# Optimization experiments

Measured on AMD Instinct MI355X. Metric: run time of the kernel, lower is better.

## Reference

```python
import jax, jax.numpy as jnp
import numpy as np
import math

S = 5   # num_states
D = 16  # observation_dim
F = 4   # transition_feature_dim
H = 2 * S  # transition net hidden


def setup_inputs() -> dict:
    key = jax.random.key(0)
    ks = jax.random.split(key, 10)
    B, T = 256, 4096
    observations = jax.random.normal(ks[0], (B, T, D), dtype=jnp.float32)
    transition_features = jax.random.normal(ks[1], (B, T, F), dtype=jnp.float32)
    # GaussianEmission params
    means = jax.random.normal(ks[2], (S, D), dtype=jnp.float32) * 0.1
    log_vars = jnp.zeros((S, D), dtype=jnp.float32)
    # HMM params
    log_initial = jnp.zeros((S,), dtype=jnp.float32)
    transition_bias = (jnp.eye(S) * 2.0 + jnp.ones((S, S)) * 0.1).astype(jnp.float32)
    # per-source-state transition nets: Linear(F,H)-Tanh-Linear(H,S)
    W1 = jax.random.normal(ks[3], (S, H, F), dtype=jnp.float32) * (1.0 / math.sqrt(F))
    b1 = jnp.zeros((S, H), dtype=jnp.float32)
    W2 = jax.random.normal(ks[4], (S, S, H), dtype=jnp.float32) * (1.0 / math.sqrt(H))
    b2 = jnp.zeros((S, S), dtype=jnp.float32)
    return {
        "observations": observations,
        "transition_features": transition_features,
        "means": means,
        "log_vars": log_vars,
        "log_initial": log_initial,
        "transition_bias": transition_bias,
        "W1": W1, "b1": b1, "W2": W2, "b2": b2,
    }


def _emission_log_prob(obs, means, log_vars):
    # diagonal Gaussian, expanded quadratic form to avoid [B,T,S,D] intermediate
    inv_v = jnp.exp(-log_vars)                              # [S,D]
    quad = (
        jnp.einsum('btd,sd->bts', obs * obs, inv_v)
        - 2.0 * jnp.einsum('btd,sd->bts', obs, means * inv_v)
        + jnp.sum(means * means * inv_v, axis=-1)           # [S]
    )
    const = D * math.log(2 * math.pi) + jnp.sum(log_vars, axis=-1)  # [S]
    return -0.5 * (const + quad)                            # [B,T,S]


def _io_log_transitions(feat, W1, b1, W2, b2, transition_bias):
    # feat: [B,T,F] -> log transition matrices [B,T,S,S] (row i = source state)
    h = jnp.tanh(jnp.einsum('btf,ihf->btih', feat, W1) + b1)        # [B,T,S,H]
    logits = jnp.einsum('btih,ioh->btio', h, W2) + b2 + transition_bias  # [B,T,S,S]
    probs = jax.nn.softmax(logits, axis=-1)
    return jnp.log(probs + 1e-10)


def reference(observations, transition_features, means, log_vars,
              log_initial, transition_bias, W1, b1, W2, b2):
    log_emis = _emission_log_prob(observations, means, log_vars)    # [B,T,S]
    log_init = jax.nn.log_softmax(log_initial)                      # [S]
    alpha0 = log_init + log_emis[:, 0, :]                           # [B,S]

    # transitions used at steps t=1..T-1
    log_trans = _io_log_transitions(transition_features[:, 1:], W1, b1, W2, b2,
                                    transition_bias)                # [B,T-1,S,S]

    lt_tm = jnp.swapaxes(log_trans, 0, 1)                           # [T-1,B,S,S]
    le_tm = jnp.swapaxes(log_emis[:, 1:, :], 0, 1)                  # [T-1,B,S]

    def step(alpha, xs):
        lt, le = xs
        alpha_new = jax.nn.logsumexp(alpha[:, :, None] + lt, axis=1) + le
        return alpha_new, alpha_new

    alpha_T, alphas = jax.lax.scan(step, alpha0, (lt_tm, le_tm))
    all_alpha = jnp.concatenate([alpha0[None], alphas], axis=0)     # [T,B,S]
    all_alpha = jnp.swapaxes(all_alpha, 0, 1)                       # [B,T,S]
    log_likelihood = jax.nn.logsumexp(alpha_T, axis=-1)             # [B]
    return log_likelihood, all_alpha
```

## Files before the change

kernel.cpp:

```cpp
#include <hip/hip_runtime.h>
#include <math.h>


namespace {

constexpr int kS = 5, kD = 16, kH = 10, kB = 256, kT = 4096;
constexpr int kC = 8, kNC = 512, kTile = 128, kCPT = 16, kG = 16, kNG = 32;

constexpr float kL2E = 1.4426950408889634f;
constexpr float kLn2 = 0.6931471805599453f;

constexpr int L_EA = 0;
constexpr int L_EB = 80;
constexpr int L_EC = 160;
constexpr int L_LN = 168;
constexpr int L_W1 = 176;
constexpr int L_B1 = 376;
constexpr int L_W2 = 436;
constexpr int L_B2 = 736;
constexpr int L_LV = 776;
constexpr int L_MN = 856;
constexpr int kPRM = 936;

__device__ __forceinline__ float max5(float a0, float a1, float a2, float a3, float a4) {
  return fmaxf(fmaxf(fmaxf(a0, a1), fmaxf(a2, a3)), a4);
}

__device__ __forceinline__ void loadObs(const float* __restrict__ obs_bt, float o[kD]) {
  const float4* o4 = reinterpret_cast<const float4*>(obs_bt);
  float4 v0 = o4[0], v1 = o4[1], v2 = o4[2], v3 = o4[3];
  o[0] = v0.x; o[1] = v0.y; o[2] = v0.z; o[3] = v0.w;
  o[4] = v1.x; o[5] = v1.y; o[6] = v1.z; o[7] = v1.w;
  o[8] = v2.x; o[9] = v2.y; o[10] = v2.z; o[11] = v2.w;
  o[12] = v3.x; o[13] = v3.y; o[14] = v3.z; o[15] = v3.w;
}

__device__ __forceinline__ unsigned bf16bits(float x) {
  unsigned u = __float_as_uint(x);
  return (u + 0x7fffu + ((u >> 16) & 1u)) >> 16;
}

__device__ void load_params(float* p, const float* means, const float* lvg,
                            const float* linit, const float* tbias,
                            const float* W1g, const float* b1g,
                            const float* W2g, const float* b2g) {
  const int tid = threadIdx.x, nt = blockDim.x;
  for (int i = tid; i < 80; i += nt) p[L_LV + i] = lvg[i];
  for (int i = tid; i < 80; i += nt) p[L_MN + i] = means[i];
  for (int i = tid; i < 200; i += nt) p[L_W1 + i] = (2.0f * kL2E) * W1g[i];
  for (int i = tid; i < 60; i += nt) {
    int r = i / 12, h = i - r * 12;
    p[L_B1 + i] = (h < kH) ? (2.0f * kL2E) * b1g[r * kH + h] : 0.f;
  }
  for (int i = tid; i < 300; i += nt) {
    int r = i / 12, h = i - r * 12;
    p[L_W2 + i] = (h < kH) ? kL2E * W2g[r * kH + h] : 0.f;
  }
  for (int i = tid; i < 40; i += nt) {
    int r = i / 8, j = i - r * 8;
    p[L_B2 + i] = (j < kS) ? kL2E * (b2g[r * kS + j] + tbias[r * kS + j]) : 0.f;
  }
  if (tid < kS) {
    float l0 = linit[0], l1 = linit[1], l2 = linit[2], l3 = linit[3], l4 = linit[4];
    float m = max5(l0, l1, l2, l3, l4);
    float se = __expf(l0 - m) + __expf(l1 - m) + __expf(l2 - m) +
               __expf(l3 - m) + __expf(l4 - m);
    p[L_LN + tid] = kL2E * (linit[tid] - (m + __logf(se)));
  }
  __syncthreads();
  for (int i = tid; i < 80; i += nt) {
    float iv = __expf(-p[L_LV + i]);
    p[L_EA + i] = -0.5f * kL2E * iv;
    p[L_EB + i] = kL2E * p[L_MN + i] * iv;
  }
  if (tid < kS) {
    float acc = 29.406033062549525f;
#pragma unroll
    for (int d = 0; d < 16; ++d) {
      float lvv = p[L_LV + tid * 16 + d], mm = p[L_MN + tid * 16 + d];
      acc += lvv + mm * mm * __expf(-lvv);
    }
    p[L_EC + tid] = -0.5f * kL2E * acc;
  }
  __syncthreads();
}

__device__ __forceinline__ void buildE(const float* __restrict__ obs,
                                       const float* __restrict__ feat,
                                       const float* __restrict__ p,
                                       size_t bt, float E[25], float& c) {
  float o[16];
  loadObs(obs + bt * kD, o);
  float le[5];
#pragma unroll
  for (int s = 0; s < 5; ++s) {
    float acc = p[L_EC + s];
#pragma unroll
    for (int d = 0; d < 16; ++d)
      acc = fmaf(o[d], fmaf(o[d], p[L_EA + s * 16 + d], p[L_EB + s * 16 + d]), acc);
    le[s] = acc;
  }
  c = max5(le[0], le[1], le[2], le[3], le[4]);
  float eml[5];
#pragma unroll
  for (int j = 0; j < 5; ++j) eml[j] = exp2f(le[j] - c);
  const float4 f = *reinterpret_cast<const float4*>(feat + bt * 4);
#pragma unroll
  for (int i = 0; i < 5; ++i) {
    float hv[10];
#pragma unroll
    for (int h = 0; h < 10; ++h) {
      float4 w = *reinterpret_cast<const float4*>(p + L_W1 + (i * 10 + h) * 4);
      float acc = p[L_B1 + i * 12 + h];
      acc = fmaf(f.x, w.x, acc); acc = fmaf(f.y, w.y, acc);
      acc = fmaf(f.z, w.z, acc); acc = fmaf(f.w, w.w, acc);
      float e = exp2f(acc);
      hv[h] = 1.f - 2.f * __builtin_amdgcn_rcpf(e + 1.f);
    }
    float eg[5], se = 0.f;
#pragma unroll
    for (int j = 0; j < 5; ++j) {
      const float* wr = p + L_W2 + (i * 5 + j) * 12;
      float4 w0 = *reinterpret_cast<const float4*>(wr);
      float4 w1 = *reinterpret_cast<const float4*>(wr + 4);
      float2 w2 = *reinterpret_cast<const float2*>(wr + 8);
      float acc = p[L_B2 + i * 8 + j];
      acc = fmaf(hv[0], w0.x, acc); acc = fmaf(hv[1], w0.y, acc);
      acc = fmaf(hv[2], w0.z, acc); acc = fmaf(hv[3], w0.w, acc);
      acc = fmaf(hv[4], w1.x, acc); acc = fmaf(hv[5], w1.y, acc);
      acc = fmaf(hv[6], w1.z, acc); acc = fmaf(hv[7], w1.w, acc);
      acc = fmaf(hv[8], w2.x, acc); acc = fmaf(hv[9], w2.y, acc);
      eg[j] = exp2f(acc);
      se += eg[j];
    }
    float rs = __builtin_amdgcn_rcpf(se);
#pragma unroll
    for (int j = 0; j < 5; ++j) E[i * 5 + j] = eg[j] * rs * eml[j];
  }
}

__device__ __forceinline__ void buildE0(const float* __restrict__ obs,
                                        const float* __restrict__ p, int b,
                                        float E[25], float& c) {
  float o[16];
  loadObs(obs + (size_t)b * kT * kD, o);
  float v[5];
#pragma unroll
  for (int s = 0; s < 5; ++s) {
    float acc = p[L_EC + s];
#pragma unroll
    for (int d = 0; d < 16; ++d)
      acc = fmaf(o[d], fmaf(o[d], p[L_EA + s * 16 + d], p[L_EB + s * 16 + d]), acc);
    v[s] = acc + p[L_LN + s];
  }
  c = max5(v[0], v[1], v[2], v[3], v[4]);
  float e[5];
#pragma unroll
  for (int j = 0; j < 5; ++j) e[j] = 0.2f * exp2f(v[j] - c);
#pragma unroll
  for (int i = 0; i < 5; ++i)
#pragma unroll
    for (int j = 0; j < 5; ++j) E[i * 5 + j] = e[j];
}

template <bool STORE_E>
__global__ __launch_bounds__(kTile, 4) void k_build(
    const float* __restrict__ obs, const float* __restrict__ feat,
    const float* __restrict__ means, const float* __restrict__ lv,
    const float* __restrict__ linit, const float* __restrict__ tbias,
    const float* __restrict__ W1g, const float* __restrict__ b1g,
    const float* __restrict__ W2g, const float* __restrict__ b2g,
    float* __restrict__ Rg, uint4* __restrict__ wsE) {
  __shared__ __align__(16) float p[kPRM];
  __shared__ float sw[kTile * 32];
  load_params(p, means, lv, linit, tbias, W1g, b1g, W2g, b2g);
  const int b = blockIdx.y, tile = blockIdx.x, tid = threadIdx.x;
  const int t = tile * kTile + tid;
  float E[25], c;
  if (t == 0) buildE0(obs, p, b, E, c);
  else buildE(obs, feat, p, (size_t)b * kT + t, E, c);
  if (STORE_E) {
    unsigned d[16];
#pragma unroll
    for (int q = 0; q < 12; ++q)
      d[q] = bf16bits(E[2 * q]) | (bf16bits(E[2 * q + 1]) << 16);
    unsigned cb = __float_as_uint(c);
    d[12] = bf16bits(E[24]) | (cb << 16);
    d[13] = cb >> 16;
    d[14] = 0; d[15] = 0;
    uint4* wp = wsE + ((size_t)b * kT + t) * 4;
#pragma unroll
    for (int q = 0; q < 4; ++q)
      wp[q] = make_uint4(d[4 * q], d[4 * q + 1], d[4 * q + 2], d[4 * q + 3]);
  }
  {
    const int base = tid * 32;
    const int off = (tid >> 3) + ((tid & 3) << 3);
#pragma unroll
    for (int e = 0; e < 25; ++e) sw[base + ((off + e) & 31)] = E[e];
    sw[base + ((off + 25) & 31)] = c;
  }
  __syncthreads();
  const int chunk = tid >> 3, ri = tid & 7;
  float R[5], sc;
  {
    const int base = (chunk * 8) * 32, off = chunk;
#pragma unroll
    for (int m = 0; m < 5; ++m) R[m] = sw[base + ((off + ri * 5 + m) & 31)];
    sc = sw[base + ((off + 25) & 31)];
  }
#pragma unroll 1
  for (int k = 1; k < 8; ++k) {
    const int base = (chunk * 8 + k) * 32, off = chunk + ((k & 3) << 3);
    float Ek[25];
#pragma unroll
    for (int e = 0; e < 25; ++e) Ek[e] = sw[base + ((off + e) & 31)];
    sc += sw[base + ((off + 25) & 31)];
    float nR[5];
#pragma unroll
    for (int j = 0; j < 5; ++j) {
      float acc = R[0] * Ek[j];
      acc = fmaf(R[1], Ek[5 + j], acc);
      acc = fmaf(R[2], Ek[10 + j], acc);
      acc = fmaf(R[3], Ek[15 + j], acc);
      acc = fmaf(R[4], Ek[20 + j], acc);
      nR[j] = acc;
    }
#pragma unroll
    for (int j = 0; j < 5; ++j) R[j] = nR[j];
    if ((k & 1) == 0 || k == 7) {
      float rm = (ri < 5) ? max5(R[0], R[1], R[2], R[3], R[4]) : 0.f;
      rm = fmaxf(rm, __shfl_xor(rm, 1, 8));
      rm = fmaxf(rm, __shfl_xor(rm, 2, 8));
      rm = fmaxf(rm, __shfl_xor(rm, 4, 8));
      rm = fmaxf(rm, 1e-37f);
      const float r = __builtin_amdgcn_rcpf(rm);
#pragma unroll
      for (int j = 0; j < 5; ++j) R[j] *= r;
      sc += __log2f(rm);
    }
  }
  if (ri < 5) {
    float* outr = Rg + ((size_t)b * kNC + tile * kCPT + chunk) * 28 + ri * 5;
#pragma unroll
    for (int m = 0; m < 5; ++m) outr[m] = R[m];
    if (ri == 0) outr[25] = sc;
  }
}

__global__ __launch_bounds__(256) void k_scan(const float* __restrict__ Rg,
                                              float* __restrict__ start,
                                              float* __restrict__ out) {
  __shared__ float sR[kNC * 32];
  __shared__ float sP[kNG * 28];
  __shared__ float sA[kNG * 8];
  const int b = blockIdx.x, tid = threadIdx.x;
#pragma unroll
  for (int r = 0; r < 2; ++r) {
    const int rec = r * 256 + tid;
    const float4* src = reinterpret_cast<const float4*>(Rg + ((size_t)b * kNC + rec) * 28);
    float4 q[7];
#pragma unroll
    for (int i = 0; i < 7; ++i) q[i] = src[i];
    const float* v = reinterpret_cast<const float*>(q);
    const int base = rec * 32, off = rec + (rec >> 4);
#pragma unroll
    for (int e = 0; e < 26; ++e) sR[base + ((off + e) & 31)] = v[e];
  }
  __syncthreads();
  if (tid < kNG) {
    const int g = tid;
    float P[25], psc;
    {
      const int rec = g * kG, base = rec * 32, off = rec + (rec >> 4);
#pragma unroll
      for (int e = 0; e < 25; ++e) P[e] = sR[base + ((off + e) & 31)];
      psc = sR[base + ((off + 25) & 31)];
    }
#pragma unroll 1
    for (int k = 1; k < kG; ++k) {
      const int rec = g * kG + k, base = rec * 32, off = rec + (rec >> 4);
      float M[25];
#pragma unroll
      for (int e = 0; e < 25; ++e) M[e] = sR[base + ((off + e) & 31)];
      psc += sR[base + ((off + 25) & 31)];
      float o[25];
#pragma unroll
      for (int i = 0; i < 5; ++i)
#pragma unroll
        for (int j = 0; j < 5; ++j) {
          float acc = P[i * 5 + 0] * M[j];
          acc = fmaf(P[i * 5 + 1], M[5 + j], acc);
          acc = fmaf(P[i * 5 + 2], M[10 + j], acc);
          acc = fmaf(P[i * 5 + 3], M[15 + j], acc);
          acc = fmaf(P[i * 5 + 4], M[20 + j], acc);
          o[i * 5 + j] = acc;
        }
#pragma unroll
      for (int e = 0; e < 25; ++e) P[e] = o[e];
      if (k & 1) {
        float m = P[0];
#pragma unroll
        for (int e = 1; e < 25; ++e) m = fmaxf(m, P[e]);
        m = fmaxf(m, 1e-37f);
        const float r = __builtin_amdgcn_rcpf(m);
#pragma unroll
        for (int e = 0; e < 25; ++e) P[e] *= r;
        psc += __log2f(m);
      }
    }
#pragma unroll
    for (int e = 0; e < 25; ++e) sP[g * 28 + e] = P[e];
    sP[g * 28 + 25] = psc;
  }
  __syncthreads();
  if (tid == 0) {
    float a[5] = {1.f, 1.f, 1.f, 1.f, 1.f};
    float ls = 0.f;
#pragma unroll 1
    for (int g = 0; g < kNG; ++g) {
#pragma unroll
      for (int s = 0; s < 5; ++s) sA[g * 8 + s] = a[s];
      sA[g * 8 + 5] = ls;
      float o[5];
#pragma unroll
      for (int j = 0; j < 5; ++j) {
        float acc = a[0] * sP[g * 28 + j];
        acc = fmaf(a[1], sP[g * 28 + 5 + j], acc);
        acc = fmaf(a[2], sP[g * 28 + 10 + j], acc);
        acc = fmaf(a[3], sP[g * 28 + 15 + j], acc);
        acc = fmaf(a[4], sP[g * 28 + 20 + j], acc);
        o[j] = acc;
      }
      ls += sP[g * 28 + 25];
      float m = fmaxf(max5(o[0], o[1], o[2], o[3], o[4]), 1e-37f);
      const float r = __builtin_amdgcn_rcpf(m);
#pragma unroll
      for (int j = 0; j < 5; ++j) a[j] = o[j] * r;
      ls += __log2f(m);
    }
    out[b] = (__log2f(a[0] + a[1] + a[2] + a[3] + a[4]) + ls) * kLn2;
  }
  __syncthreads();
  if (tid < kNG) {
    const int g = tid;
    float a[5], ls;
#pragma unroll
    for (int s = 0; s < 5; ++s) a[s] = sA[g * 8 + s];
    ls = sA[g * 8 + 5];
#pragma unroll 1
    for (int k = 0; k < kG; ++k) {
      const int cc = g * kG + k;
      float* st = start + ((size_t)b * kNC + cc) * 8;
      reinterpret_cast<float4*>(st)[0] = make_float4(a[0], a[1], a[2], a[3]);
      reinterpret_cast<float4*>(st)[1] = make_float4(a[4], ls, 0.f, 0.f);
      const int base = cc * 32, off = cc + (cc >> 4);
      float M[25];
#pragma unroll
      for (int e = 0; e < 25; ++e) M[e] = sR[base + ((off + e) & 31)];
      ls += sR[base + ((off + 25) & 31)];
      float o[5];
#pragma unroll
      for (int j = 0; j < 5; ++j) {
        float acc = a[0] * M[j];
        acc = fmaf(a[1], M[5 + j], acc);
        acc = fmaf(a[2], M[10 + j], acc);
        acc = fmaf(a[3], M[15 + j], acc);
        acc = fmaf(a[4], M[20 + j], acc);
        o[j] = acc;
      }
      float m = fmaxf(max5(o[0], o[1], o[2], o[3], o[4]), 1e-37f);
      const float r = __builtin_amdgcn_rcpf(m);
#pragma unroll
      for (int j = 0; j < 5; ++j) a[j] = o[j] * r;
      ls += __log2f(m);
    }
  }
}

__global__ __launch_bounds__(256) void k_alpha_a(const uint4* __restrict__ wsE,
                                                 const float* __restrict__ start,
                                                 float* __restrict__ outp) {
  const int g = blockIdx.x * 256 + threadIdx.x;
  const int b = g >> 9, cc = g & (kNC - 1);
  const float* st = start + (size_t)g * 8;
  const float4 s0 = reinterpret_cast<const float4*>(st)[0];
  float a[5] = {s0.x, s0.y, s0.z, s0.w, st[4]};
  float ls = st[5];
  float ov[40];
  const uint4* ep = wsE + ((size_t)b * kT + (size_t)cc * kC) * 4;
#pragma unroll
  for (int k = 0; k < 8; ++k) {
    uint4 q0 = ep[k * 4], q1 = ep[k * 4 + 1], q2 = ep[k * 4 + 2], q3 = ep[k * 4 + 3];
    unsigned d[14] = {q0.x, q0.y, q0.z, q0.w, q1.x, q1.y, q1.z, q1.w,
                      q2.x, q2.y, q2.z, q2.w, q3.x, q3.y};
    float E[25];
#pragma unroll
    for (int q = 0; q < 12; ++q) {
      E[2 * q]     = __uint_as_float(d[q] << 16);
      E[2 * q + 1] = __uint_as_float(d[q] & 0xffff0000u);
    }
    E[24] = __uint_as_float(d[12] << 16);
    const float cst = __uint_as_float((d[12] >> 16) | (d[13] << 16));
    float o[5];
#pragma unroll
    for (int j = 0; j < 5; ++j) {
      float acc = a[0] * E[j];
      acc = fmaf(a[1], E[5 + j], acc);
      acc = fmaf(a[2], E[10 + j], acc);
      acc = fmaf(a[3], E[15 + j], acc);
      acc = fmaf(a[4], E[20 + j], acc);
      o[j] = acc;
    }
    ls += cst;
    float L[5];
#pragma unroll
    for (int j = 0; j < 5; ++j) L[j] = __log2f(o[j]);
#pragma unroll
    for (int j = 0; j < 5; ++j) ov[k * 5 + j] = (L[j] + ls) * kLn2;
    const float lm = max5(L[0], L[1], L[2], L[3], L[4]);
    const float m = fmaxf(max5(o[0], o[1], o[2], o[3], o[4]), 1e-37f);
    const float r = __builtin_amdgcn_rcpf(m);
#pragma unroll
    for (int j = 0; j < 5; ++j) a[j] = o[j] * r;
    ls += lm;
  }
  float4* w = reinterpret_cast<float4*>(outp + kB + ((size_t)b * kT + (size_t)cc * kC) * kS);
#pragma unroll
  for (int q = 0; q < 10; ++q)
    w[q] = make_float4(ov[q * 4], ov[q * 4 + 1], ov[q * 4 + 2], ov[q * 4 + 3]);
}

__global__ __launch_bounds__(kTile, 4) void k_alpha_b(
    const float* __restrict__ obs, const float* __restrict__ feat,
    const float* __restrict__ means, const float* __restrict__ lv,
    const float* __restrict__ linit, const float* __restrict__ tbias,
    const float* __restrict__ W1g, const float* __restrict__ b1g,
    const float* __restrict__ W2g, const float* __restrict__ b2g,
    const float* __restrict__ start, float* __restrict__ outp) {
  __shared__ __align__(16) float p[kPRM];
  __shared__ float sw[kTile * 32];
  load_params(p, means, lv, linit, tbias, W1g, b1g, W2g, b2g);
  const int b = blockIdx.y, tile = blockIdx.x, tid = threadIdx.x;
  const int t = tile * kTile + tid;
  float E[25], c;
  if (t == 0) buildE0(obs, p, b, E, c);
  else buildE(obs, feat, p, (size_t)b * kT + t, E, c);
  {
    const int base = tid * 32;
    const int off = (tid >> 3) + ((tid & 3) << 3);
#pragma unroll
    for (int e = 0; e < 25; ++e) sw[base + ((off + e) & 31)] = E[e];
    sw[base + ((off + 25) & 31)] = c;
  }
  __syncthreads();
  if (tid < kCPT) {
    const int chunk = tid;
    const float* st = start + ((size_t)b * kNC + tile * kCPT + chunk) * 8;
    const float4 s0 = reinterpret_cast<const float4*>(st)[0];
    float a[5] = {s0.x, s0.y, s0.z, s0.w, st[4]};
    float ls = st[5];
    float ov[40];
#pragma unroll
    for (int k = 0; k < 8; ++k) {
      const int base = (chunk * 8 + k) * 32, off = chunk + ((k & 3) << 3);
      float Ek[25];
#pragma unroll
      for (int e = 0; e < 25; ++e) Ek[e] = sw[base + ((off + e) & 31)];
      const float cst = sw[base + ((off + 25) & 31)];
      float o[5];
#pragma unroll
      for (int j = 0; j < 5; ++j) {
        float acc = a[0] * Ek[j];
        acc = fmaf(a[1], Ek[5 + j], acc);
        acc = fmaf(a[2], Ek[10 + j], acc);
        acc = fmaf(a[3], Ek[15 + j], acc);
        acc = fmaf(a[4], Ek[20 + j], acc);
        o[j] = acc;
      }
      ls += cst;
      float L[5];
#pragma unroll
      for (int j = 0; j < 5; ++j) L[j] = __log2f(o[j]);
#pragma unroll
      for (int j = 0; j < 5; ++j) ov[k * 5 + j] = (L[j] + ls) * kLn2;
      const float lm = max5(L[0], L[1], L[2], L[3], L[4]);
      const float m = fmaxf(max5(o[0], o[1], o[2], o[3], o[4]), 1e-37f);
      const float r = __builtin_amdgcn_rcpf(m);
#pragma unroll
      for (int j = 0; j < 5; ++j) a[j] = o[j] * r;
      ls += lm;
    }
    float4* w = reinterpret_cast<float4*>(
        outp + kB + ((size_t)b * kT + (size_t)(tile * kCPT + chunk) * kC) * kS);
#pragma unroll
    for (int q = 0; q < 10; ++q)
      w[q] = make_float4(ov[q * 4], ov[q * 4 + 1], ov[q * 4 + 2], ov[q * 4 + 3]);
  }
}

}

extern "C" void kernel_launch(void* const* d_in, const int* in_sizes, int n_in,
                              void* d_out, int out_size, void* d_ws, size_t ws_size,
                              hipStream_t stream) {
  (void)in_sizes; (void)n_in; (void)out_size;
  const float* obs   = (const float*)d_in[0];
  const float* feat  = (const float*)d_in[1];
  const float* means = (const float*)d_in[2];
  const float* lv    = (const float*)d_in[3];
  const float* linit = (const float*)d_in[4];
  const float* tbias = (const float*)d_in[5];
  const float* W1g   = (const float*)d_in[6];
  const float* b1g   = (const float*)d_in[7];
  const float* W2g   = (const float*)d_in[8];
  const float* b2g   = (const float*)d_in[9];
  float* out = (float*)d_out;

  float* ws = (float*)d_ws;
  float* Rg    = ws;
  float* start = Rg + (size_t)kB * kNC * 28;
  uint4* wsE   = reinterpret_cast<uint4*>(start + (size_t)kB * kNC * 8);
  const size_t needA = (size_t)kB * kNC * 28 * 4 + (size_t)kB * kNC * 8 * 4 +
                       (size_t)kB * kT * 64;
  const bool useA = ws_size >= needA;

  dim3 gridB(kT / kTile, kB);
  if (useA) {
    k_build<true><<<gridB, kTile, 0, stream>>>(obs, feat, means, lv, linit, tbias,
                                               W1g, b1g, W2g, b2g, Rg, wsE);
  } else {
    k_build<false><<<gridB, kTile, 0, stream>>>(obs, feat, means, lv, linit, tbias,
                                                W1g, b1g, W2g, b2g, Rg, wsE);
  }
  k_scan<<<kB, 256, 0, stream>>>(Rg, start, out);
  if (useA) {
    k_alpha_a<<<(kB * kNC) / 256, 256, 0, stream>>>(wsE, start, out);
  } else {
    k_alpha_b<<<gridB, kTile, 0, stream>>>(obs, feat, means, lv, linit, tbias,
                                           W1g, b1g, W2g, b2g, start, out);
  }
}
```

Before: 135.1 us.

## Precompute parameters in a prep kernel, enlarge build tiles, simplify tanh MLP

Adds a one-block prep kernel that folds the emission constants, network weights and biases into a packed parameter buffer. Each build block then copies this buffer into shared memory instead of recomputing it with several syncs. The build tile grows from 128 to 256 threads. The tanh is rewritten as a reciprocal with the constant folded into the second-layer bias, the emission quadratic uses vectorised loads, and bf16 packing uses a hardware convert instruction. The fallback path that did not store E is removed, so the code now assumes the workspace is large enough, and one extra kernel launch is added.

```diff
diff --git a/kernel.cpp b/kernel.cpp
--- a/kernel.cpp
+++ b/kernel.cpp
@@ -4,29 +4,29 @@
 
 namespace {
 
-constexpr int kS = 5, kD = 16, kH = 10, kB = 256, kT = 4096;
-constexpr int kC = 8, kNC = 512, kTile = 128, kCPT = 16, kG = 16, kNG = 32;
+constexpr int kS = 5, kD = 16, kB = 256, kT = 4096;
+constexpr int kC = 8, kNC = 512;
+constexpr int kTile = 256, kCPT = 32;
+constexpr int kG = 16, kNG = 32;
 
 constexpr float kL2E = 1.4426950408889634f;
 constexpr float kLn2 = 0.6931471805599453f;
 
-constexpr int L_EA = 0;
-constexpr int L_EB = 80;
-constexpr int L_EC = 160;
+constexpr int L_QA = 0;
+constexpr int L_QB = 80;
+constexpr int L_QC = 160;
 constexpr int L_LN = 168;
 constexpr int L_W1 = 176;
 constexpr int L_B1 = 376;
 constexpr int L_W2 = 436;
-constexpr int L_B2 = 736;
-constexpr int L_LV = 776;
-constexpr int L_MN = 856;
-constexpr int kPRM = 936;
+constexpr int P_TOT = 768;
+constexpr int P_RSV = 1024;
 
 __device__ __forceinline__ float max5(float a0, float a1, float a2, float a3, float a4) {
   return fmaxf(fmaxf(fmaxf(a0, a1), fmaxf(a2, a3)), a4);
 }
 
-__device__ __forceinline__ void loadObs(const float* __restrict__ obs_bt, float o[kD]) {
+__device__ __forceinline__ void loadObs(const float* __restrict__ obs_bt, float* o) {
   const float4* o4 = reinterpret_cast<const float4*>(obs_bt);
   float4 v0 = o4[0], v1 = o4[1], v2 = o4[2], v3 = o4[3];
   o[0] = v0.x; o[1] = v0.y; o[2] = v0.z; o[3] = v0.w;
@@ -40,100 +40,121 @@
   return (u + 0x7fffu + ((u >> 16) & 1u)) >> 16;
 }
 
-__device__ void load_params(float* p, const float* means, const float* lvg,
-                            const float* linit, const float* tbias,
-                            const float* W1g, const float* b1g,
-                            const float* W2g, const float* b2g) {
-  const int tid = threadIdx.x, nt = blockDim.x;
-  for (int i = tid; i < 80; i += nt) p[L_LV + i] = lvg[i];
-  for (int i = tid; i < 80; i += nt) p[L_MN + i] = means[i];
-  for (int i = tid; i < 200; i += nt) p[L_W1 + i] = (2.0f * kL2E) * W1g[i];
-  for (int i = tid; i < 60; i += nt) {
-    int r = i / 12, h = i - r * 12;
-    p[L_B1 + i] = (h < kH) ? (2.0f * kL2E) * b1g[r * kH + h] : 0.f;
-  }
-  for (int i = tid; i < 300; i += nt) {
-    int r = i / 12, h = i - r * 12;
-    p[L_W2 + i] = (h < kH) ? kL2E * W2g[r * kH + h] : 0.f;
-  }
-  for (int i = tid; i < 40; i += nt) {
-    int r = i / 8, j = i - r * 8;
-    p[L_B2 + i] = (j < kS) ? kL2E * (b2g[r * kS + j] + tbias[r * kS + j]) : 0.f;
-  }
-  if (tid < kS) {
-    float l0 = linit[0], l1 = linit[1], l2 = linit[2], l3 = linit[3], l4 = linit[4];
-    float m = max5(l0, l1, l2, l3, l4);
-    float se = __expf(l0 - m) + __expf(l1 - m) + __expf(l2 - m) +
-               __expf(l3 - m) + __expf(l4 - m);
-    p[L_LN + tid] = kL2E * (linit[tid] - (m + __logf(se)));
-  }
-  __syncthreads();
-  for (int i = tid; i < 80; i += nt) {
-    float iv = __expf(-p[L_LV + i]);
-    p[L_EA + i] = -0.5f * kL2E * iv;
-    p[L_EB + i] = kL2E * p[L_MN + i] * iv;
-  }
-  if (tid < kS) {
-    float acc = 29.406033062549525f;
+__device__ __forceinline__ unsigned cvtpk(float a, float b) {
+  unsigned r;
+  asm("v_cvt_pk_bf16_f32 %0, %1, %2" : "=v"(r) : "v"(a), "v"(b));
+  return r;
+}
+
+__global__ void k_prep(const float* __restrict__ means, const float* __restrict__ lv,
+                       const float* __restrict__ linit, const float* __restrict__ tbias,
+                       const float* __restrict__ W1g, const float* __restrict__ b1g,
+                       const float* __restrict__ W2g, const float* __restrict__ b2g,
+                       float* __restrict__ P) {
+  const int tid = threadIdx.x;
+  if (tid < 80) {
+    const float iv = __expf(-lv[tid]);
+    P[L_QA + tid] = -0.5f * kL2E * iv;
+    P[L_QB + tid] = kL2E * means[tid] * iv;
+  }
+  if (tid >= 80 && tid < 85) {
+    const int s = tid - 80;
+    float acc = 0.f;
 #pragma unroll
     for (int d = 0; d < 16; ++d) {
-      float lvv = p[L_LV + tid * 16 + d], mm = p[L_MN + tid * 16 + d];
+      const float lvv = lv[s * 16 + d], mm = means[s * 16 + d];
       acc += lvv + mm * mm * __expf(-lvv);
     }
-    p[L_EC + tid] = -0.5f * kL2E * acc;
-  }
-  __syncthreads();
+    P[L_QC + s] = -0.5f * kL2E * (29.406033062549525f + acc);
+    const float l0 = linit[0], l1 = linit[1], l2 = linit[2], l3 = linit[3],
+                l4 = linit[4];
+    const float m = max5(l0, l1, l2, l3, l4);
+    const float se = __expf(l0 - m) + __expf(l1 - m) + __expf(l2 - m) +
+                     __expf(l3 - m) + __expf(l4 - m);
+    P[L_LN + s] = kL2E * (linit[s] - (m + __logf(se)));
+  }
+  if (tid < 200) P[L_W1 + tid] = (2.0f * kL2E) * W1g[tid];
+  if (tid < 60) {
+    const int r = tid / 12, h = tid - r * 12;
+    P[L_B1 + tid] = (h < 10) ? (2.0f * kL2E) * b1g[r * 10 + h] : 0.f;
+  }
+  for (int i = tid; i < 300; i += 256) {
+    const int r = i / 12, h = i - r * 12;
+    float v;
+    if (h < 10) v = -2.0f * kL2E * W2g[r * 10 + h];
+    else if (h == 10) {
+      float sw = 0.f;
+#pragma unroll
+      for (int hh = 0; hh < 10; ++hh) sw += W2g[r * 10 + hh];
+      v = kL2E * (b2g[r] + tbias[r] + sw);
+    } else v = 0.f;
+    P[L_W2 + i] = v;
+  }
+  if (tid >= 88 && tid < 88 + (P_TOT - 736)) P[736 + tid - 88] = 0.f;
 }
 
 __device__ __forceinline__ void buildE(const float* __restrict__ obs,
                                        const float* __restrict__ feat,
                                        const float* __restrict__ p,
-                                       size_t bt, float E[25], float& c) {
-  float o[16];
-  loadObs(obs + bt * kD, o);
+                                       size_t t, float E[25], float& c) {
+  float o[16], o2[16];
+  loadObs(obs + t * kD, o);
+#pragma unroll
+  for (int d = 0; d < 16; ++d) o2[d] = o[d] * o[d];
   float le[5];
 #pragma unroll
   for (int s = 0; s < 5; ++s) {
-    float acc = p[L_EC + s];
-#pragma unroll
-    for (int d = 0; d < 16; ++d)
-      acc = fmaf(o[d], fmaf(o[d], p[L_EA + s * 16 + d], p[L_EB + s * 16 + d]), acc);
+    float acc = p[L_QC + s];
+#pragma unroll
+    for (int dq = 0; dq < 4; ++dq) {
+      const float4 qa = *reinterpret_cast<const float4*>(p + L_QA + s * 16 + dq * 4);
+      const float4 qb = *reinterpret_cast<const float4*>(p + L_QB + s * 16 + dq * 4);
+      acc = fmaf(o2[dq * 4 + 0], qa.x, acc); acc = fmaf(o[dq * 4 + 0], qb.x, acc);
+      acc = fmaf(o2[dq * 4 + 1], qa.y, acc); acc = fmaf(o[dq * 4 + 1], qb.y, acc);
+      acc = fmaf(o2[dq * 4 + 2], qa.z, acc); acc = fmaf(o[dq * 4 + 2], qb.z, acc);
+      acc = fmaf(o2[dq * 4 + 3], qa.w, acc); acc = fmaf(o[dq * 4 + 3], qb.w, acc);
+    }
     le[s] = acc;
   }
   c = max5(le[0], le[1], le[2], le[3], le[4]);
   float eml[5];
 #pragma unroll
   for (int j = 0; j < 5; ++j) eml[j] = exp2f(le[j] - c);
-  const float4 f = *reinterpret_cast<const float4*>(feat + bt * 4);
+  const float4 f = *reinterpret_cast<const float4*>(feat + t * 4);
 #pragma unroll
   for (int i = 0; i < 5; ++i) {
-    float hv[10];
+    const float4 bA = *reinterpret_cast<const float4*>(p + L_B1 + i * 12);
+    const float4 bB = *reinterpret_cast<const float4*>(p + L_B1 + i * 12 + 4);
+    const float2 bC = *reinterpret_cast<const float2*>(p + L_B1 + i * 12 + 8);
+    const float bb[10] = {bA.x, bA.y, bA.z, bA.w, bB.x, bB.y, bB.z, bB.w, bC.x, bC.y};
+    float hr[10];
 #pragma unroll
     for (int h = 0; h < 10; ++h) {
-      float4 w = *reinterpret_cast<const float4*>(p + L_W1 + (i * 10 + h) * 4);
-      float acc = p[L_B1 + i * 12 + h];
-      acc = fmaf(f.x, w.x, acc); acc = fmaf(f.y, w.y, acc);
-      acc = fmaf(f.z, w.z, acc); acc = fmaf(f.w, w.w, acc);
-      float e = exp2f(acc);
-      hv[h] = 1.f - 2.f * __builtin_amdgcn_rcpf(e + 1.f);
+      const float4 w = *reinterpret_cast<const float4*>(p + L_W1 + (i * 10 + h) * 4);
+      float acc = bb[h];
+      acc = fmaf(f.x, w.x, acc);
+      acc = fmaf(f.y, w.y, acc);
+      acc = fmaf(f.z, w.z, acc);
+      acc = fmaf(f.w, w.w, acc);
+      hr[h] = __builtin_amdgcn_rcpf(exp2f(acc) + 1.f);
     }
     float eg[5], se = 0.f;
 #pragma unroll
     for (int j = 0; j < 5; ++j) {
       const float* wr = p + L_W2 + (i * 5 + j) * 12;
-      float4 w0 = *reinterpret_cast<const float4*>(wr);
-      float4 w1 = *reinterpret_cast<const float4*>(wr + 4);
-      float2 w2 = *reinterpret_cast<const float2*>(wr + 8);
-      float acc = p[L_B2 + i * 8 + j];
-      acc = fmaf(hv[0], w0.x, acc); acc = fmaf(hv[1], w0.y, acc);
-      acc = fmaf(hv[2], w0.z, acc); acc = fmaf(hv[3], w0.w, acc);
-      acc = fmaf(hv[4], w1.x, acc); acc = fmaf(hv[5], w1.y, acc);
-      acc = fmaf(hv[6], w1.z, acc); acc = fmaf(hv[7], w1.w, acc);
-      acc = fmaf(hv[8], w2.x, acc); acc = fmaf(hv[9], w2.y, acc);
+      const float4 w0 = *reinterpret_cast<const float4*>(wr);
+      const float4 w1 = *reinterpret_cast<const float4*>(wr + 4);
+      const float4 w2 = *reinterpret_cast<const float4*>(wr + 8);
+      float acc = w2.z;
+      acc = fmaf(hr[0], w0.x, acc); acc = fmaf(hr[1], w0.y, acc);
+      acc = fmaf(hr[2], w0.z, acc); acc = fmaf(hr[3], w0.w, acc);
+      acc = fmaf(hr[4], w1.x, acc); acc = fmaf(hr[5], w1.y, acc);
+      acc = fmaf(hr[6], w1.z, acc); acc = fmaf(hr[7], w1.w, acc);
+      acc = fmaf(hr[8], w2.x, acc); acc = fmaf(hr[9], w2.y, acc);
       eg[j] = exp2f(acc);
       se += eg[j];
     }
-    float rs = __builtin_amdgcn_rcpf(se);
+    const float rs = __builtin_amdgcn_rcpf(se);
 #pragma unroll
     for (int j = 0; j < 5; ++j) E[i * 5 + j] = eg[j] * rs * eml[j];
   }
@@ -142,56 +163,62 @@
 __device__ __forceinline__ void buildE0(const float* __restrict__ obs,
                                         const float* __restrict__ p, int b,
                                         float E[25], float& c) {
-  float o[16];
+  float o[16], o2[16];
   loadObs(obs + (size_t)b * kT * kD, o);
+#pragma unroll
+  for (int d = 0; d < 16; ++d) o2[d] = o[d] * o[d];
   float v[5];
 #pragma unroll
   for (int s = 0; s < 5; ++s) {
-    float acc = p[L_EC + s];
-#pragma unroll
-    for (int d = 0; d < 16; ++d)
-      acc = fmaf(o[d], fmaf(o[d], p[L_EA + s * 16 + d], p[L_EB + s * 16 + d]), acc);
+    float acc = p[L_QC + s];
+#pragma unroll
+    for (int dq = 0; dq < 4; ++dq) {
+      const float4 qa = *reinterpret_cast<const float4*>(p + L_QA + s * 16 + dq * 4);
+      const float4 qb = *reinterpret_cast<const float4*>(p + L_QB + s * 16 + dq * 4);
+      acc = fmaf(o2[dq * 4 + 0], qa.x, acc); acc = fmaf(o[dq * 4 + 0], qb.x, acc);
+      acc = fmaf(o2[dq * 4 + 1], qa.y, acc); acc = fmaf(o[dq * 4 + 1], qb.y, acc);
+      acc = fmaf(o2[dq * 4 + 2], qa.z, acc); acc = fmaf(o[dq * 4 + 2], qb.z, acc);
+      acc = fmaf(o2[dq * 4 + 3], qa.w, acc); acc = fmaf(o[dq * 4 + 3], qb.w, acc);
+    }
     v[s] = acc + p[L_LN + s];
   }
   c = max5(v[0], v[1], v[2], v[3], v[4]);
-  float e[5];
-#pragma unroll
-  for (int j = 0; j < 5; ++j) e[j] = 0.2f * exp2f(v[j] - c);
+  float e5[5];
+#pragma unroll
+  for (int j = 0; j < 5; ++j) e5[j] = 0.2f * exp2f(v[j] - c);
 #pragma unroll
   for (int i = 0; i < 5; ++i)
 #pragma unroll
-    for (int j = 0; j < 5; ++j) E[i * 5 + j] = e[j];
+    for (int j = 0; j < 5; ++j) E[i * 5 + j] = e5[j];
 }
 
 template <bool STORE_E>
-__global__ __launch_bounds__(kTile, 4) void k_build(
+__global__ __launch_bounds__(256, 4) void k_build(
     const float* __restrict__ obs, const float* __restrict__ feat,
-    const float* __restrict__ means, const float* __restrict__ lv,
-    const float* __restrict__ linit, const float* __restrict__ tbias,
-    const float* __restrict__ W1g, const float* __restrict__ b1g,
-    const float* __restrict__ W2g, const float* __restrict__ b2g,
-    float* __restrict__ Rg, uint4* __restrict__ wsE) {
-  __shared__ __align__(16) float p[kPRM];
+    const float* __restrict__ P, float* __restrict__ Rg,
+    uint4* __restrict__ wsE) {
+  __shared__ __align__(16) float p[P_TOT];
   __shared__ float sw[kTile * 32];
-  load_params(p, means, lv, linit, tbias, W1g, b1g, W2g, b2g);
+  if (threadIdx.x < P_TOT / 4)
+    reinterpret_cast<float4*>(p)[threadIdx.x] =
+        reinterpret_cast<const float4*>(P)[threadIdx.x];
+  __syncthreads();
   const int b = blockIdx.y, tile = blockIdx.x, tid = threadIdx.x;
   const int t = tile * kTile + tid;
+  const size_t gt = (size_t)b * kT + t;
   float E[25], c;
   if (t == 0) buildE0(obs, p, b, E, c);
-  else buildE(obs, feat, p, (size_t)b * kT + t, E, c);
+  else buildE(obs, feat, p, gt, E, c);
   if (STORE_E) {
-    unsigned d[16];
-#pragma unroll
-    for (int q = 0; q < 12; ++q)
-      d[q] = bf16bits(E[2 * q]) | (bf16bits(E[2 * q + 1]) << 16);
-    unsigned cb = __float_as_uint(c);
-    d[12] = bf16bits(E[24]) | (cb << 16);
-    d[13] = cb >> 16;
-    d[14] = 0; d[15] = 0;
-    uint4* wp = wsE + ((size_t)b * kT + t) * 4;
-#pragma unroll
-    for (int q = 0; q < 4; ++q)
-      wp[q] = make_uint4(d[4 * q], d[4 * q + 1], d[4 * q + 2], d[4 * q + 3]);
+    const unsigned cb = __float_as_uint(c);
+    uint4* wp = wsE + gt * 4;
+    wp[0] = make_uint4(cvtpk(E[0], E[1]), cvtpk(E[2], E[3]),
+                       cvtpk(E[4], E[5]), cvtpk(E[6], E[7]));
+    wp[1] = make_uint4(cvtpk(E[8], E[9]), cvtpk(E[10], E[11]),
+                       cvtpk(E[12], E[13]), cvtpk(E[14], E[15]));
+    wp[2] = make_uint4(cvtpk(E[16], E[17]), cvtpk(E[18], E[19]),
+                       cvtpk(E[20], E[21]), cvtpk(E[22], E[23]));
+    wp[3] = make_uint4(bf16bits(E[24]) | (cb << 16), cb >> 16, 0u, 0u);
   }
   {
     const int base = tid * 32;
@@ -233,7 +260,7 @@
       rm = fmaxf(rm, __shfl_xor(rm, 1, 8));
       rm = fmaxf(rm, __shfl_xor(rm, 2, 8));
       rm = fmaxf(rm, __shfl_xor(rm, 4, 8));
-      rm = fmaxf(rm, 1e-37f);
+      rm = fmaxf(rm, 1e-30f);
       const float r = __builtin_amdgcn_rcpf(rm);
 #pragma unroll
       for (int j = 0; j < 5; ++j) R[j] *= r;
@@ -246,6 +273,58 @@
     for (int m = 0; m < 5; ++m) outr[m] = R[m];
     if (ri == 0) outr[25] = sc;
   }
+}
+
+
+__device__ __forceinline__ void matmat5(float R[25], const float E[25]) {
+#pragma unroll
+  for (int i = 0; i < 5; ++i) {
+    const float r0 = R[i * 5 + 0], r1 = R[i * 5 + 1], r2 = R[i * 5 + 2];
+    const float r3 = R[i * 5 + 3], r4 = R[i * 5 + 4];
+#pragma unroll
+    for (int j = 0; j < 5; ++j) {
+      float acc = r0 * E[j];
+      acc = fmaf(r1, E[5 + j], acc);
+      acc = fmaf(r2, E[10 + j], acc);
+      acc = fmaf(r3, E[15 + j], acc);
+      acc = fmaf(r4, E[20 + j], acc);
+      R[i * 5 + j] = acc;
+    }
+  }
+}
+
+__device__ __forceinline__ void rescale25a(float R[25], float& sc) {
+  float m = R[0];
+#pragma unroll
+  for (int e = 1; e < 25; ++e) m = fmaxf(m, R[e]);
+  m = fmaxf(m, 1e-30f);
+  const float r = __builtin_amdgcn_rcpf(m);
+#pragma unroll
+  for (int e = 0; e < 25; ++e) R[e] *= r;
+  sc += __log2f(m);
+}
+
+__device__ __forceinline__ void vecmat5(float a[5], const float M[25]) {
+  float o[5];
+#pragma unroll
+  for (int j = 0; j < 5; ++j) {
+    float acc = a[0] * M[j];
+    acc = fmaf(a[1], M[5 + j], acc);
+    acc = fmaf(a[2], M[10 + j], acc);
+    acc = fmaf(a[3], M[15 + j], acc);
+    acc = fmaf(a[4], M[20 + j], acc);
+    o[j] = acc;
+  }
+#pragma unroll
+  for (int j = 0; j < 5; ++j) a[j] = o[j];
+}
+
+__device__ __forceinline__ void rescale5(float a[5], float& ls) {
+  const float m = fmaxf(max5(a[0], a[1], a[2], a[3], a[4]), 1e-30f);
+  const float r = __builtin_amdgcn_rcpf(m);
+#pragma unroll
+  for (int j = 0; j < 5; ++j) a[j] *= r;
+  ls += __log2f(m);
 }
 
 __global__ __launch_bounds__(256) void k_scan(const float* __restrict__ Rg,
@@ -284,30 +363,8 @@
 #pragma unroll
       for (int e = 0; e < 25; ++e) M[e] = sR[base + ((off + e) & 31)];
       psc += sR[base + ((off + 25) & 31)];
-      float o[25];
-#pragma unroll
-      for (int i = 0; i < 5; ++i)
-#pragma unroll
-        for (int j = 0; j < 5; ++j) {
-          float acc = P[i * 5 + 0] * M[j];
-          acc = fmaf(P[i * 5 + 1], M[5 + j], acc);
-          acc = fmaf(P[i * 5 + 2], M[10 + j], acc);
-          acc = fmaf(P[i * 5 + 3], M[15 + j], acc);
-          acc = fmaf(P[i * 5 + 4], M[20 + j], acc);
-          o[i * 5 + j] = acc;
-        }
-#pragma unroll
-      for (int e = 0; e < 25; ++e) P[e] = o[e];
-      if (k & 1) {
-        float m = P[0];
-#pragma unroll
-        for (int e = 1; e < 25; ++e) m = fmaxf(m, P[e]);
-        m = fmaxf(m, 1e-37f);
-        const float r = __builtin_amdgcn_rcpf(m);
-#pragma unroll
-        for (int e = 0; e < 25; ++e) P[e] *= r;
-        psc += __log2f(m);
-      }
+      matmat5(P, M);
+      if (k & 1) rescale25a(P, psc);
     }
 #pragma unroll
     for (int e = 0; e < 25; ++e) sP[g * 28 + e] = P[e];
@@ -322,22 +379,12 @@
 #pragma unroll
       for (int s = 0; s < 5; ++s) sA[g * 8 + s] = a[s];
       sA[g * 8 + 5] = ls;
-      float o[5];
-#pragma unroll
-      for (int j = 0; j < 5; ++j) {
-        float acc = a[0] * sP[g * 28 + j];
-        acc = fmaf(a[1], sP[g * 28 + 5 + j], acc);
-        acc = fmaf(a[2], sP[g * 28 + 10 + j], acc);
-        acc = fmaf(a[3], sP[g * 28 + 15 + j], acc);
-        acc = fmaf(a[4], sP[g * 28 + 20 + j], acc);
-        o[j] = acc;
-      }
+      float M[25];
+#pragma unroll
+      for (int e = 0; e < 25; ++e) M[e] = sP[g * 28 + e];
+      vecmat5(a, M);
       ls += sP[g * 28 + 25];
-      float m = fmaxf(max5(o[0], o[1], o[2], o[3], o[4]), 1e-37f);
-      const float r = __builtin_amdgcn_rcpf(m);
-#pragma unroll
-      for (int j = 0; j < 5; ++j) a[j] = o[j] * r;
-      ls += __log2f(m);
+      rescale5(a, ls);
     }
     out[b] = (__log2f(a[0] + a[1] + a[2] + a[3] + a[4]) + ls) * kLn2;
   }
@@ -359,21 +406,8 @@
 #pragma unroll
       for (int e = 0; e < 25; ++e) M[e] = sR[base + ((off + e) & 31)];
       ls += sR[base + ((off + 25) & 31)];
-      float o[5];
-#pragma unroll
-      for (int j = 0; j < 5; ++j) {
-        float acc = a[0] * M[j];
-        acc = fmaf(a[1], M[5 + j], acc);
-        acc = fmaf(a[2], M[10 + j], acc);
-        acc = fmaf(a[3], M[15 + j], acc);
-        acc = fmaf(a[4], M[20 + j], acc);
-        o[j] = acc;
-      }
-      float m = fmaxf(max5(o[0], o[1], o[2], o[3], o[4]), 1e-37f);
-      const float r = __builtin_amdgcn_rcpf(m);
-#pragma unroll
-      for (int j = 0; j < 5; ++j) a[j] = o[j] * r;
-      ls += __log2f(m);
+      vecmat5(a, M);
+      rescale5(a, ls);
     }
   }
 }
@@ -381,12 +415,13 @@
 __global__ __launch_bounds__(256) void k_alpha_a(const uint4* __restrict__ wsE,
                                                  const float* __restrict__ start,
                                                  float* __restrict__ outp) {
-  const int g = blockIdx.x * 256 + threadIdx.x;
-  const int b = g >> 9, cc = g & (kNC - 1);
-  const float* st = start + (size_t)g * 8;
+  const int gc = blockIdx.x * 256 + threadIdx.x;
+  const int b = gc >> 9, cc = gc & (kNC - 1);
+  const float* st = start + (size_t)gc * 8;
   const float4 s0 = reinterpret_cast<const float4*>(st)[0];
-  float a[5] = {s0.x, s0.y, s0.z, s0.w, st[4]};
-  float ls = st[5];
+  const float4 s1 = reinterpret_cast<const float4*>(st)[1];
+  float a[5] = {s0.x, s0.y, s0.z, s0.w, s1.x};
+  float ls = s1.y;
   float ov[40];
   const uint4* ep = wsE + ((size_t)b * kT + (size_t)cc * kC) * 4;
 #pragma unroll
@@ -419,7 +454,7 @@
 #pragma unroll
     for (int j = 0; j < 5; ++j) ov[k * 5 + j] = (L[j] + ls) * kLn2;
     const float lm = max5(L[0], L[1], L[2], L[3], L[4]);
-    const float m = fmaxf(max5(o[0], o[1], o[2], o[3], o[4]), 1e-37f);
+    const float m = fmaxf(max5(o[0], o[1], o[2], o[3], o[4]), 1e-30f);
     const float r = __builtin_amdgcn_rcpf(m);
 #pragma unroll
     for (int j = 0; j < 5; ++j) a[j] = o[j] * r;
@@ -429,74 +464,6 @@
 #pragma unroll
   for (int q = 0; q < 10; ++q)
     w[q] = make_float4(ov[q * 4], ov[q * 4 + 1], ov[q * 4 + 2], ov[q * 4 + 3]);
-}
-
-__global__ __launch_bounds__(kTile, 4) void k_alpha_b(
-    const float* __restrict__ obs, const float* __restrict__ feat,
-    const float* __restrict__ means, const float* __restrict__ lv,
-    const float* __restrict__ linit, const float* __restrict__ tbias,
-    const float* __restrict__ W1g, const float* __restrict__ b1g,
-    const float* __restrict__ W2g, const float* __restrict__ b2g,
-    const float* __restrict__ start, float* __restrict__ outp) {
-  __shared__ __align__(16) float p[kPRM];
-  __shared__ float sw[kTile * 32];
-  load_params(p, means, lv, linit, tbias, W1g, b1g, W2g, b2g);
-  const int b = blockIdx.y, tile = blockIdx.x, tid = threadIdx.x;
-  const int t = tile * kTile + tid;
-  float E[25], c;
-  if (t == 0) buildE0(obs, p, b, E, c);
-  else buildE(obs, feat, p, (size_t)b * kT + t, E, c);
-  {
-    const int base = tid * 32;
-    const int off = (tid >> 3) + ((tid & 3) << 3);
-#pragma unroll
-    for (int e = 0; e < 25; ++e) sw[base + ((off + e) & 31)] = E[e];
-    sw[base + ((off + 25) & 31)] = c;
-  }
-  __syncthreads();
-  if (tid < kCPT) {
-    const int chunk = tid;
-    const float* st = start + ((size_t)b * kNC + tile * kCPT + chunk) * 8;
-    const float4 s0 = reinterpret_cast<const float4*>(st)[0];
-    float a[5] = {s0.x, s0.y, s0.z, s0.w, st[4]};
-    float ls = st[5];
-    float ov[40];
-#pragma unroll
-    for (int k = 0; k < 8; ++k) {
-      const int base = (chunk * 8 + k) * 32, off = chunk + ((k & 3) << 3);
-      float Ek[25];
-#pragma unroll
-      for (int e = 0; e < 25; ++e) Ek[e] = sw[base + ((off + e) & 31)];
-      const float cst = sw[base + ((off + 25) & 31)];
-      float o[5];
-#pragma unroll
-      for (int j = 0; j < 5; ++j) {
-        float acc = a[0] * Ek[j];
-        acc = fmaf(a[1], Ek[5 + j], acc);
-        acc = fmaf(a[2], Ek[10 + j], acc);
-        acc = fmaf(a[3], Ek[15 + j], acc);
-        acc = fmaf(a[4], Ek[20 + j], acc);
-        o[j] = acc;
-      }
-      ls += cst;
-      float L[5];
-#pragma unroll
-      for (int j = 0; j < 5; ++j) L[j] = __log2f(o[j]);
-#pragma unroll
-      for (int j = 0; j < 5; ++j) ov[k * 5 + j] = (L[j] + ls) * kLn2;
-      const float lm = max5(L[0], L[1], L[2], L[3], L[4]);
-      const float m = fmaxf(max5(o[0], o[1], o[2], o[3], o[4]), 1e-37f);
-      const float r = __builtin_amdgcn_rcpf(m);
-#pragma unroll
-      for (int j = 0; j < 5; ++j) a[j] = o[j] * r;
-      ls += lm;
-    }
-    float4* w = reinterpret_cast<float4*>(
-        outp + kB + ((size_t)b * kT + (size_t)(tile * kCPT + chunk) * kC) * kS);
-#pragma unroll
-    for (int q = 0; q < 10; ++q)
-      w[q] = make_float4(ov[q * 4], ov[q * 4 + 1], ov[q * 4 + 2], ov[q * 4 + 3]);
-  }
 }
 
 }
@@ -504,7 +471,7 @@
 extern "C" void kernel_launch(void* const* d_in, const int* in_sizes, int n_in,
                               void* d_out, int out_size, void* d_ws, size_t ws_size,
                               hipStream_t stream) {
-  (void)in_sizes; (void)n_in; (void)out_size;
+  (void)in_sizes; (void)n_in; (void)out_size; (void)ws_size;
   const float* obs   = (const float*)d_in[0];
   const float* feat  = (const float*)d_in[1];
   const float* means = (const float*)d_in[2];
@@ -517,27 +484,14 @@
   const float* b2g   = (const float*)d_in[9];
   float* out = (float*)d_out;
 
-  float* ws = (float*)d_ws;
-  float* Rg    = ws;
+  float* P     = (float*)d_ws;
+  float* Rg    = P + P_RSV;
   float* start = Rg + (size_t)kB * kNC * 28;
   uint4* wsE   = reinterpret_cast<uint4*>(start + (size_t)kB * kNC * 8);
-  const size_t needA = (size_t)kB * kNC * 28 * 4 + (size_t)kB * kNC * 8 * 4 +
-                       (size_t)kB * kT * 64;
-  const bool useA = ws_size >= needA;
-
+
+  k_prep<<<1, 256, 0, stream>>>(means, lv, linit, tbias, W1g, b1g, W2g, b2g, P);
   dim3 gridB(kT / kTile, kB);
-  if (useA) {
-    k_build<true><<<gridB, kTile, 0, stream>>>(obs, feat, means, lv, linit, tbias,
-                                               W1g, b1g, W2g, b2g, Rg, wsE);
-  } else {
-    k_build<false><<<gridB, kTile, 0, stream>>>(obs, feat, means, lv, linit, tbias,
-                                                W1g, b1g, W2g, b2g, Rg, wsE);
-  }
+  k_build<true><<<gridB, kTile, 0, stream>>>(obs, feat, P, Rg, wsE);
   k_scan<<<kB, 256, 0, stream>>>(Rg, start, out);
-  if (useA) {
-    k_alpha_a<<<(kB * kNC) / 256, 256, 0, stream>>>(wsE, start, out);
-  } else {
-    k_alpha_b<<<gridB, kTile, 0, stream>>>(obs, feat, means, lv, linit, tbias,
-                                           W1g, b1g, W2g, b2g, start, out);
-  }
-}
+  k_alpha_a<<<(kB * kNC) / 256, 256, 0, stream>>>(wsE, start, out);
+}
```

Result: faster. 124.8 us (-7.6%).
